# Kernel tuning notes

Measured on AMD Instinct MI355X. Metric: run time of the kernel, lower is better.

## Reference

```python
import jax, jax.numpy as jnp
import numpy as np

B, L, H, E, M = 8, 1024, 1024, 2048, 2048  # batch, seq, hidden_dim, expanded_dim, max_seq_length


def setup_inputs() -> dict:
    key = jax.random.key(0)
    ks = jax.random.split(key, 10)
    n = lambda k, shape, s=0.02: jax.random.normal(k, shape, jnp.float32) * s
    return {
        'x': jax.random.normal(ks[0], (B, L, H), jnp.float32),
        'ln1_w': jnp.ones((H,), jnp.float32), 'ln1_b': jnp.zeros((H,), jnp.float32),
        'ln2_w': jnp.ones((E,), jnp.float32), 'ln2_b': jnp.zeros((E,), jnp.float32),
        'w_qkv': n(ks[1], (3 * E, H)), 'b_qkv': jnp.zeros((3 * E,), jnp.float32),
        'w_out': n(ks[2], (H, E)), 'b_out': jnp.zeros((H,), jnp.float32),
        'rel_pos': n(ks[3], (2 * M - 1, H)),
        'w_beta': n(ks[4], (E, 2 * H)), 'b_beta': jnp.zeros((E,), jnp.float32),
        'w1': n(ks[5], (4 * H, H)), 'b1': jnp.zeros((4 * H,), jnp.float32),
        'w2': n(ks[6], (H, 4 * H)), 'b2': jnp.zeros((H,), jnp.float32),
        'conv_w': n(ks[7], (E, 1, 3), 0.3),  # depthwise conv1d weight [C,1,K]
        'attn_scale': jnp.ones((1,), jnp.float32),
    }


def _ln(x, w, b):
    m = jnp.mean(x, -1, keepdims=True)
    v = jnp.mean((x - m) ** 2, -1, keepdims=True)
    return (x - m) / jnp.sqrt(v + 1e-5) * w + b


def _normalize(x):
    # F.normalize(x, dim=-1): x / max(||x||_2, 1e-12)
    return x / jnp.maximum(jnp.linalg.norm(x, axis=-1, keepdims=True), 1e-12)


def _dwconv(z, w):
    # z: [B,L,E]; depthwise conv1d k=3, pad=1, no bias (groups=E)
    y = jax.lax.conv_general_dilated(
        z.transpose(0, 2, 1), w, window_strides=(1,), padding=((1, 1),),
        feature_group_count=w.shape[0], dimension_numbers=('NCH', 'OIH', 'NCH'))
    return y.transpose(0, 2, 1)


def reference(x, ln1_w, ln1_b, ln2_w, ln2_b, w_qkv, b_qkv, w_out, b_out,
              rel_pos, w_beta, b_beta, w1, b1, w2, b2, conv_w, attn_scale):
    Lx = x.shape[1]
    h = _ln(x, ln1_w, ln1_b)
    qkv = h @ w_qkv.T + b_qkv
    q, k, v = jnp.split(qkv, 3, axis=-1)  # each [B,L,E]
    q = jax.nn.silu(q)
    k = jax.nn.silu(k)
    v = jax.nn.gelu(v, approximate=False)
    # interdependent normalize-mix (k uses the updated q)
    q = _normalize(q) + 0.1 * k
    k = _normalize(k) + 0.1 * q
    q = _dwconv(q, conv_w)
    k = _dwconv(k, conv_w)
    v = _dwconv(v, conv_w)
    # position-conditioned beta gate
    pos_embed = rel_pos[:Lx]  # [L,H]
    pos_info = jnp.einsum('blh,mh->blm', h, pos_embed).mean(-1, keepdims=True)  # [B,L,1]
    comb = jnp.concatenate([h, jnp.broadcast_to(pos_info, h.shape)], axis=-1)  # [B,L,2H]
    beta = jax.nn.sigmoid(comb @ w_beta.T + b_beta) * 0.9 + 0.1  # [B,L,E]
    # delta-rule: state starts at zeros so v_old = state @ k^T = 0 exactly
    v_new = beta * v  # beta*v + (1-beta)*0
    state = jnp.einsum('ble,blf->bef', v_new, k)  # v_new^T @ k : [B,E,E]
    out = jnp.einsum('ble,bfe->blf', q, state) * attn_scale  # q @ state^T
    out = _ln(out, ln2_w, ln2_b) @ w_out.T + b_out
    x = x + out
    h2 = _ln(x, ln1_w, ln1_b)  # norm1 is reused pre-MLP
    mlp = jax.nn.gelu(h2 @ w1.T + b1, approximate=False) @ w2.T + b2
    return x + mlp
```

## Files before the change

### kernel.cpp

```cpp
#include <hip/hip_runtime.h>
#include <hip/hip_bf16.h>
#include <math.h>

using bf16 = __hip_bfloat16;
typedef __attribute__((ext_vector_type(8))) short bf16x8;
typedef __attribute__((ext_vector_type(4))) float f32x4;

#define DEVI __device__ __forceinline__

DEVI float b2f(bf16 v) { return __bfloat162float(v); }
DEVI bf16 f2b(float v) { return __float2bfloat16(v); }
DEVI float geluf(float x) { return 0.5f * x * (1.0f + erff(x * 0.70710678118654752f)); }
DEVI float siluf(float x) { return x / (1.0f + expf(-x)); }

DEVI void load_lds16(const bf16* g, bf16* l) {
  __builtin_amdgcn_global_load_lds(
      (const __attribute__((address_space(1))) void*)g,
      (__attribute__((address_space(3))) void*)l, 16, 0, 0);
}

__global__ __launch_bounds__(256) void cast_kernel(const float* __restrict__ in,
                                                   bf16* __restrict__ out, int n4) {
  int i = blockIdx.x * 256 + threadIdx.x;
  if (i >= n4) return;
  float4 v = reinterpret_cast<const float4*>(in)[i];
  bf16 o[4] = { f2b(v.x), f2b(v.y), f2b(v.z), f2b(v.w) };
  reinterpret_cast<uint2*>(out)[i] = *reinterpret_cast<uint2*>(o);
}

__global__ __launch_bounds__(256) void prep_kernel(const float* __restrict__ rel,
                                                   float* __restrict__ pm,
                                                   const float* __restrict__ wb,
                                                   float* __restrict__ wb2s) {
  const int b = blockIdx.x;
  if (b < 4) {
    int h = b * 256 + threadIdx.x;
    float s = 0.f;
    for (int m = 0; m < 1024; ++m) s += rel[m * 1024 + h];
    pm[h] = s * (1.0f / 1024.0f);
  } else {
    int e = (b - 4) * 4 + (threadIdx.x >> 6);
    int lane = threadIdx.x & 63;
    float s = 0.f;
    for (int j = lane; j < 1024; j += 64) s += wb[(long)e * 2048 + 1024 + j];
#pragma unroll
    for (int off = 32; off > 0; off >>= 1) s += __shfl_down(s, off);
    if (lane == 0) wb2s[e] = s;
  }
}

__global__ __launch_bounds__(256) void convw_pack_kernel(const float* __restrict__ cw,
                                                         bf16* __restrict__ wpl) {
  int e = blockIdx.x * 256 + threadIdx.x;
  wpl[e]        = f2b(cw[e * 3]);
  wpl[2048 + e] = f2b(cw[e * 3 + 1]);
  wpl[4096 + e] = f2b(cw[e * 3 + 2]);
}

template<bool POS>
__global__ __launch_bounds__(256) void ln1024_kernel(
    const float* __restrict__ x, const float* __restrict__ w, const float* __restrict__ b,
    bf16* __restrict__ out, const float* __restrict__ pmean, float* __restrict__ pos) {
  __shared__ float red[12];
  long row = blockIdx.x;
  int t = threadIdx.x, lane = t & 63, wid = t >> 6;
  float4 xv = reinterpret_cast<const float4*>(x + row * 1024)[t];
  float s = xv.x + xv.y + xv.z + xv.w;
  float ss = xv.x * xv.x + xv.y * xv.y + xv.z * xv.z + xv.w * xv.w;
#pragma unroll
  for (int off = 32; off > 0; off >>= 1) { s += __shfl_down(s, off); ss += __shfl_down(ss, off); }
  if (lane == 0) { red[wid] = s; red[4 + wid] = ss; }
  __syncthreads();
  s = red[0] + red[1] + red[2] + red[3];
  ss = red[4] + red[5] + red[6] + red[7];
  float mean = s * (1.0f / 1024.0f);
  float rstd = rsqrtf(ss * (1.0f / 1024.0f) - mean * mean + 1e-5f);
  float4 wv = reinterpret_cast<const float4*>(w)[t];
  float4 bv = reinterpret_cast<const float4*>(b)[t];
  float h0 = (xv.x - mean) * rstd * wv.x + bv.x;
  float h1 = (xv.y - mean) * rstd * wv.y + bv.y;
  float h2 = (xv.z - mean) * rstd * wv.z + bv.z;
  float h3 = (xv.w - mean) * rstd * wv.w + bv.w;
  bf16 o[4] = { f2b(h0), f2b(h1), f2b(h2), f2b(h3) };
  reinterpret_cast<uint2*>(out + row * 1024)[t] = *reinterpret_cast<uint2*>(o);
  if (POS) {
    float4 pv = reinterpret_cast<const float4*>(pmean)[t];
    float d = h0 * pv.x + h1 * pv.y + h2 * pv.z + h3 * pv.w;
#pragma unroll
    for (int off = 32; off > 0; off >>= 1) d += __shfl_down(d, off);
    if (lane == 0) red[8 + wid] = d;
    __syncthreads();
    if (t == 0) pos[row] = red[8] + red[9] + red[10] + red[11];
  }
}

__global__ __launch_bounds__(256) void ln1024b_kernel(
    const bf16* __restrict__ x, const float* __restrict__ w, const float* __restrict__ b,
    bf16* __restrict__ out) {
  __shared__ float red[8];
  long row = blockIdx.x;
  int t = threadIdx.x, lane = t & 63, wid = t >> 6;
  bf16 tv[4];
  *reinterpret_cast<uint2*>(tv) = reinterpret_cast<const uint2*>(x + row * 1024)[t];
  float v[4], s = 0.f, ss = 0.f;
#pragma unroll
  for (int j = 0; j < 4; ++j) { v[j] = b2f(tv[j]); s += v[j]; ss += v[j] * v[j]; }
#pragma unroll
  for (int off = 32; off > 0; off >>= 1) { s += __shfl_down(s, off); ss += __shfl_down(ss, off); }
  if (lane == 0) { red[wid] = s; red[4 + wid] = ss; }
  __syncthreads();
  s = red[0] + red[1] + red[2] + red[3];
  ss = red[4] + red[5] + red[6] + red[7];
  float mean = s * (1.0f / 1024.0f);
  float rstd = rsqrtf(ss * (1.0f / 1024.0f) - mean * mean + 1e-5f);
  float4 wv = reinterpret_cast<const float4*>(w)[t];
  float4 bv = reinterpret_cast<const float4*>(b)[t];
  bf16 o[4];
  o[0] = f2b((v[0] - mean) * rstd * wv.x + bv.x);
  o[1] = f2b((v[1] - mean) * rstd * wv.y + bv.y);
  o[2] = f2b((v[2] - mean) * rstd * wv.z + bv.z);
  o[3] = f2b((v[3] - mean) * rstd * wv.w + bv.w);
  reinterpret_cast<uint2*>(out + row * 1024)[t] = *reinterpret_cast<uint2*>(o);
}

__global__ __launch_bounds__(256) void ln2048_bf16_kernel(
    const bf16* __restrict__ in, const float* __restrict__ w, const float* __restrict__ b,
    bf16* __restrict__ out) {
  __shared__ float red[8];
  long row = blockIdx.x;
  int t = threadIdx.x, lane = t & 63, wid = t >> 6;
  bf16 tv[8];
  *reinterpret_cast<int4*>(tv) = reinterpret_cast<const int4*>(in + row * 2048)[t];
  float v[8], s = 0.f, ss = 0.f;
#pragma unroll
  for (int j = 0; j < 8; ++j) { v[j] = b2f(tv[j]); s += v[j]; ss += v[j] * v[j]; }
#pragma unroll
  for (int off = 32; off > 0; off >>= 1) { s += __shfl_down(s, off); ss += __shfl_down(ss, off); }
  if (lane == 0) { red[wid] = s; red[4 + wid] = ss; }
  __syncthreads();
  s = red[0] + red[1] + red[2] + red[3];
  ss = red[4] + red[5] + red[6] + red[7];
  float mean = s * (1.0f / 2048.0f);
  float rstd = rsqrtf(ss * (1.0f / 2048.0f) - mean * mean + 1e-5f);
  int base = t * 8;
  bf16 o[8];
#pragma unroll
  for (int j = 0; j < 8; ++j) o[j] = f2b((v[j] - mean) * rstd * w[base + j] + b[base + j]);
  reinterpret_cast<int4*>(out + row * 2048)[t] = *reinterpret_cast<int4*>(o);
}

__global__ __launch_bounds__(256) void act_norm_kernel(
    bf16* __restrict__ qp, bf16* __restrict__ kp, bf16* __restrict__ vp) {
  __shared__ float red[8];
  long row = blockIdx.x;
  int t = threadIdx.x, lane = t & 63, wid = t >> 6;
  long ob = row * 2048 + t * 8;
  bf16 tq[8], tk[8], tv[8];
  *reinterpret_cast<int4*>(tq) = *reinterpret_cast<const int4*>(qp + ob);
  *reinterpret_cast<int4*>(tk) = *reinterpret_cast<const int4*>(kp + ob);
  *reinterpret_cast<int4*>(tv) = *reinterpret_cast<const int4*>(vp + ob);
  float qs[8], ks[8];
  float sq = 0.f, sk = 0.f;
#pragma unroll
  for (int j = 0; j < 8; ++j) {
    float q = b2f(tq[j]); qs[j] = siluf(q); sq += qs[j] * qs[j];
    float k = b2f(tk[j]); ks[j] = siluf(k); sk += ks[j] * ks[j];
  }
#pragma unroll
  for (int off = 32; off > 0; off >>= 1) { sq += __shfl_down(sq, off); sk += __shfl_down(sk, off); }
  if (lane == 0) { red[wid] = sq; red[4 + wid] = sk; }
  __syncthreads();
  sq = red[0] + red[1] + red[2] + red[3];
  sk = red[4] + red[5] + red[6] + red[7];
  float rq = 1.0f / fmaxf(sqrtf(sq), 1e-12f);
  float rk = 1.0f / fmaxf(sqrtf(sk), 1e-12f);
  bf16 oq[8], ok[8], ov[8];
#pragma unroll
  for (int j = 0; j < 8; ++j) {
    float qn = qs[j] * rq + 0.1f * ks[j];
    float kn = ks[j] * rk + 0.1f * qn;
    oq[j] = f2b(qn); ok[j] = f2b(kn);
    ov[j] = f2b(geluf(b2f(tv[j])));
  }
  *reinterpret_cast<int4*>(qp + ob) = *reinterpret_cast<int4*>(oq);
  *reinterpret_cast<int4*>(kp + ob) = *reinterpret_cast<int4*>(ok);
  *reinterpret_cast<int4*>(vp + ob) = *reinterpret_cast<int4*>(ov);
}

__global__ __launch_bounds__(256) void dwconv2_kernel(
    const bf16* __restrict__ a_in, bf16* __restrict__ a_out,
    const bf16* __restrict__ b_in, bf16* __restrict__ b_out,
    const bf16* __restrict__ wpl) {
  const bf16* in = blockIdx.y ? b_in : a_in;
  bf16* out = blockIdx.y ? b_out : a_out;
  const int t = threadIdx.x;
  const int e0 = t * 8;
  const long bl = blockIdx.x;
  const int l = (int)(bl & 1023);
  const bf16* mid = in + (bl * 2048 + e0);
  bf16 tm[8], tp[8], tn[8], w0[8], w1[8], w2[8];
  *reinterpret_cast<int4*>(tm) = *reinterpret_cast<const int4*>(mid);
  if (l > 0)    *reinterpret_cast<int4*>(tp) = *reinterpret_cast<const int4*>(mid - 2048);
  if (l < 1023) *reinterpret_cast<int4*>(tn) = *reinterpret_cast<const int4*>(mid + 2048);
  *reinterpret_cast<int4*>(w0) = *reinterpret_cast<const int4*>(&wpl[e0]);
  *reinterpret_cast<int4*>(w1) = *reinterpret_cast<const int4*>(&wpl[2048 + e0]);
  *reinterpret_cast<int4*>(w2) = *reinterpret_cast<const int4*>(&wpl[4096 + e0]);
  bf16 o[8];
#pragma unroll
  for (int j = 0; j < 8; ++j) {
    float a = b2f(w1[j]) * b2f(tm[j]);
    if (l > 0) a += b2f(w0[j]) * b2f(tp[j]);
    if (l < 1023) a += b2f(w2[j]) * b2f(tn[j]);
    o[j] = f2b(a);
  }
  *reinterpret_cast<int4*>(out + (bl * 2048 + e0)) = *reinterpret_cast<int4*>(o);
}

__global__ __launch_bounds__(256) void transpose_kernel(const bf16* __restrict__ in,
                                                        bf16* __restrict__ out) {
  const long base = (long)blockIdx.z * 2097152;
  const int r0 = blockIdx.y * 64 + ((threadIdx.x & 63) >> 3) * 8;
  const int c0 = blockIdx.x * 256 + (threadIdx.x >> 6) * 64 + (threadIdx.x & 7) * 8;
  bf16 v[8][8];
#pragma unroll
  for (int j = 0; j < 8; ++j)
    *reinterpret_cast<int4*>(v[j]) =
        *reinterpret_cast<const int4*>(&in[base + (long)(r0 + j) * 2048 + c0]);
#pragma unroll
  for (int i = 0; i < 8; ++i) {
    bf16 w[8];
#pragma unroll
    for (int j = 0; j < 8; ++j) w[j] = v[j][i];
    *reinterpret_cast<int4*>(&out[base + (long)(c0 + i) * 1024 + r0]) =
        *reinterpret_cast<int4*>(w);
  }
}

enum { EPI_QKV = 0, EPI_BETA = 1, EPI_BF16 = 2, EPI_SCALE = 3, EPI_RES_F32 = 4, EPI_GELU = 5 };

#define MF(d, a, b) d = __builtin_amdgcn_mfma_f32_16x16x32_bf16(a, b, d, 0, 0, 0)
#define RD_A(S, MR, KK) \
  (*reinterpret_cast<const bf16x8*>(&smem[(S)*16384 + wm*8192 + ((MR)*16 + r16)*64 + ((((KK)*32) + kq8) ^ swz)]))
#define RD_B(S, NR, KK) \
  (*reinterpret_cast<const bf16x8*>(&smem[32768 + (S)*16384 + (wn>>1)*8192 + ((wn&1)*64 + (NR)*16 + r16)*64 + ((((KK)*32) + kq8) ^ swz)]))
#define STAGE_A1(S, H, Q, KT) \
  load_lds16(Abase + (long)((H)*128 + (Q)*64) * lda + (long)(KT)*64, \
             &smem[(S)*16384 + (H)*8192 + (Q)*4096 + wid*512])
#define STAGE_B1(S, H, Q, KT) \
  load_lds16(Bbase + (long)((H)*128 + (Q)*64) * ldb + (long)(KT)*64, \
             &smem[32768 + (S)*16384 + (H)*8192 + (Q)*4096 + wid*512])
#define STAGE_AH(S, H, KT) { STAGE_A1(S, H, 0, KT); STAGE_A1(S, H, 1, KT); }
#define STAGE_BH(S, H, KT) { STAGE_B1(S, H, 0, KT); STAGE_B1(S, H, 1, KT); }
#define BAR_A __builtin_amdgcn_s_barrier()
#define LGKM0 { asm volatile("s_waitcnt lgkmcnt(0)" ::: "memory"); __builtin_amdgcn_sched_barrier(0); }
#define VWAIT(LST) { if (LST) { asm volatile("s_waitcnt vmcnt(0)" ::: "memory"); } \
                     else     { asm volatile("s_waitcnt vmcnt(6)" ::: "memory"); } \
                     __builtin_amdgcn_sched_barrier(0); }

#define KTILE(S, ST1, ST2, ST3, ST4, W4) { \
  bf16x8 aL[4][2], aH[4][2], bL[2][2], bH[2][2]; \
  _Pragma("unroll") for (int m_ = 0; m_ < 4; ++m_) { aL[m_][0] = RD_A(S, m_, 0); aL[m_][1] = RD_A(S, m_, 1); } \
  _Pragma("unroll") for (int n_ = 0; n_ < 2; ++n_) { bL[n_][0] = RD_B(S, n_, 0); bL[n_][1] = RD_B(S, n_, 1); } \
  ST1; BAR_A; LGKM0; \
  __builtin_amdgcn_s_setprio(1); \
  _Pragma("unroll") for (int m_ = 0; m_ < 4; ++m_) _Pragma("unroll") for (int n_ = 0; n_ < 2; ++n_) { \
    MF(acc[m_][n_], aL[m_][0], bL[n_][0]); MF(acc[m_][n_], aL[m_][1], bL[n_][1]); } \
  __builtin_amdgcn_s_setprio(0); __builtin_amdgcn_s_barrier(); \
  _Pragma("unroll") for (int n_ = 0; n_ < 2; ++n_) { bH[n_][0] = RD_B(S, n_ + 2, 0); bH[n_][1] = RD_B(S, n_ + 2, 1); } \
  ST2; BAR_A; LGKM0; \
  __builtin_amdgcn_s_setprio(1); \
  _Pragma("unroll") for (int m_ = 0; m_ < 4; ++m_) _Pragma("unroll") for (int n_ = 0; n_ < 2; ++n_) { \
    MF(acc[m_][n_ + 2], aL[m_][0], bH[n_][0]); MF(acc[m_][n_ + 2], aL[m_][1], bH[n_][1]); } \
  __builtin_amdgcn_s_setprio(0); __builtin_amdgcn_s_barrier(); \
  _Pragma("unroll") for (int m_ = 0; m_ < 4; ++m_) { aH[m_][0] = RD_A(S, m_ + 4, 0); aH[m_][1] = RD_A(S, m_ + 4, 1); } \
  ST3; BAR_A; LGKM0; \
  __builtin_amdgcn_s_setprio(1); \
  _Pragma("unroll") for (int m_ = 0; m_ < 4; ++m_) _Pragma("unroll") for (int n_ = 0; n_ < 2; ++n_) { \
    MF(acc[m_ + 4][n_], aH[m_][0], bL[n_][0]); MF(acc[m_ + 4][n_], aH[m_][1], bL[n_][1]); } \
  __builtin_amdgcn_s_setprio(0); __builtin_amdgcn_s_barrier(); \
  ST4; W4; BAR_A; LGKM0; \
  __builtin_amdgcn_s_setprio(1); \
  _Pragma("unroll") for (int m_ = 0; m_ < 4; ++m_) _Pragma("unroll") for (int n_ = 0; n_ < 2; ++n_) { \
    MF(acc[m_ + 4][n_ + 2], aH[m_][0], bH[n_][0]); MF(acc[m_ + 4][n_ + 2], aH[m_][1], bH[n_][1]); } \
  __builtin_amdgcn_s_setprio(0); __builtin_amdgcn_s_barrier(); \
}

template<int EPI>
__global__ __launch_bounds__(512) void gemm256_kernel(
    const bf16* __restrict__ A, int lda, long sA,
    const bf16* __restrict__ B, int ldb, long sB,
    void* __restrict__ Cv, int ldc, long sC, int K,
    const float* __restrict__ bias, const float* __restrict__ aux_row,
    const float* __restrict__ aux_col, const bf16* __restrict__ vconv,
    const float* __restrict__ resid, const float* __restrict__ scale_ptr,
    bf16* __restrict__ p2, bf16* __restrict__ p3) {
  __shared__ bf16 smem[65536];
  const int bz = blockIdx.z;
  A += (long)bz * sA;
  B += (long)bz * sB;
  const int m0 = blockIdx.y * 256, n0 = blockIdx.x * 256;
  const int t = threadIdx.x, lane = t & 63, wid = t >> 6;
  const int wm = wid >> 2, wn = wid & 3;
  const int r16 = lane & 15, kq8 = (lane >> 4) * 8;
  const int swz = (r16 & 7) << 3;
  const int lrow = lane >> 3;
  const int cswz = ((lane & 7) ^ lrow) * 8;
  const bf16* Abase = A + (long)(m0 + wid * 8 + lrow) * lda + cswz;
  const bf16* Bbase = B + (long)(n0 + wid * 8 + lrow) * ldb + cswz;
  f32x4 acc[8][4] = {};
  const int NT = K >> 6, NIT = NT >> 1;
  STAGE_AH(0, 0, 0); STAGE_AH(0, 1, 0); STAGE_BH(0, 0, 0); STAGE_BH(0, 1, 0);
  STAGE_BH(1, 0, 1); STAGE_BH(1, 1, 1); STAGE_AH(1, 0, 1);
  asm volatile("s_waitcnt vmcnt(6)" ::: "memory");
  __builtin_amdgcn_sched_barrier(0);
  __builtin_amdgcn_s_barrier();
  for (int i = 0; i < NIT; ++i) {
    const int tb = 2 * i;
    const bool lst = (i == NIT - 1);
    KTILE(0,
      { STAGE_AH(1, 1, tb + 1); },
      { },
      { if (!lst) { STAGE_BH(0, 0, tb + 2); STAGE_BH(0, 1, tb + 2); } },
      { if (!lst) { STAGE_AH(0, 0, tb + 2); } },
      VWAIT(lst));
    KTILE(1,
      { if (!lst) { STAGE_AH(0, 1, tb + 2); } },
      { },
      { if (!lst) { STAGE_BH(1, 0, tb + 3); STAGE_BH(1, 1, tb + 3); } },
      { if (!lst) { STAGE_AH(1, 0, tb + 3); } },
      VWAIT(lst));
  }
  float scl = 1.0f;
  if (EPI == EPI_SCALE) scl = scale_ptr[0];
  const int rb = (lane >> 4) * 4;
#pragma unroll
  for (int mr = 0; mr < 8; ++mr) {
#pragma unroll
    for (int nr = 0; nr < 4; ++nr) {
#pragma unroll
      for (int r = 0; r < 4; ++r) {
        const long gm = m0 + wm * 128 + mr * 16 + rb + r;
        const int gn = n0 + wn * 64 + nr * 16 + r16;
        const long idx = (long)bz * sC + gm * (long)ldc + gn;
        float v = acc[mr][nr][r];
        if (EPI == EPI_QKV) {
          const int seg = gn >> 11, cc = gn & 2047;
          bf16* dst = (seg == 0) ? (bf16*)Cv : (seg == 1) ? p2 : p3;
          dst[gm * 2048 + cc] = f2b(v + bias[gn]);
        } else if (EPI == EPI_BETA) {
          float tt = v + bias[gn] + aux_row[gm] * aux_col[gn];
          float be = 0.9f / (1.0f + expf(-tt)) + 0.1f;
          ((bf16*)Cv)[idx] = f2b(be * b2f(vconv[idx]));
        } else if (EPI == EPI_BF16) {
          ((bf16*)Cv)[idx] = f2b(v);
        } else if (EPI == EPI_SCALE) {
          ((bf16*)Cv)[idx] = f2b(v * scl);
        } else if (EPI == EPI_RES_F32) {
          ((float*)Cv)[idx] = v + bias[gn] + resid[idx];
        } else {
          ((bf16*)Cv)[idx] = f2b(geluf(v + bias[gn]));
        }
      }
    }
  }
}

#define A_RD(S, MR, KK) \
  (*reinterpret_cast<const bf16x8*>(&amem[(S)*8192 + (wm*64 + (MR)*16 + r16)*64 + ((((KK)*32) + kq8) ^ swz)]))
#define B_RD(S, NR, KK) \
  (*reinterpret_cast<const bf16x8*>(&amem[16384 + (S)*16384 + (wn*64 + (NR)*16 + r16)*64 + ((((KK)*32) + kq8) ^ swz)]))
#define A_ST(S, Q, KT) \
  load_lds16(Abase + (long)((Q)*64) * lda + (long)(KT)*64, &amem[(S)*8192 + (Q)*4096 + wid*512])
#define B_ST(S, Q, KT) \
  load_lds16(Bbase + (long)((Q)*64) * ldb + (long)(KT)*64, &amem[16384 + (S)*16384 + (Q)*4096 + wid*512])
#define STAGE_T(S, KT) { A_ST(S, 0, KT); A_ST(S, 1, KT); B_ST(S, 0, KT); B_ST(S, 1, KT); B_ST(S, 2, KT); B_ST(S, 3, KT); }

template<int RB, int WB, int NR>
__global__ __launch_bounds__(512) void gemmA128_kernel(
    const bf16* __restrict__ A, int lda, long sA,
    const bf16* __restrict__ B, int ldb, long sB,
    void* __restrict__ Cv, int ldc, long sC, int K,
    const float* __restrict__ bias, const void* __restrict__ residv) {
  __shared__ bf16 amem[49152];
  A += (long)blockIdx.z * sA;
  B += (long)blockIdx.z * sB;
  const int m0 = blockIdx.y * 128, n0 = blockIdx.x * 256;
  const int t = threadIdx.x, lane = t & 63, wid = t >> 6;
  const int wm = wid >> 2, wn = wid & 3;
  const int r16 = lane & 15, kq8 = (lane >> 4) * 8;
  const int swz = (r16 & 7) << 3;
  const int lrow = lane >> 3;
  const int cswz = ((lane & 7) ^ lrow) * 8;
  const bf16* Abase = A + (long)(m0 + wid * 8 + lrow) * lda + cswz;
  const bf16* Bbase = B + (long)(n0 + wid * 8 + lrow) * ldb + cswz;
  f32x4 acc[4][4] = {};
  const int NT = K >> 6;
  STAGE_T(0, 0); STAGE_T(1, 1);
  asm volatile("s_waitcnt vmcnt(6)" ::: "memory");
  __builtin_amdgcn_sched_barrier(0);
  __builtin_amdgcn_s_barrier();
  for (int tt = 0; tt < NT; ++tt) {
    const int S = tt & 1;
    const bool pre = (tt + 2 < NT);
    bf16x8 a[4][2], bL[2][2], bH[2][2];
#pragma unroll
    for (int m_ = 0; m_ < 4; ++m_) { a[m_][0] = A_RD(S, m_, 0); a[m_][1] = A_RD(S, m_, 1); }
#pragma unroll
    for (int n_ = 0; n_ < 2; ++n_) { bL[n_][0] = B_RD(S, n_, 0); bL[n_][1] = B_RD(S, n_, 1); }
#pragma unroll
    for (int n_ = 0; n_ < 2; ++n_) { bH[n_][0] = B_RD(S, n_ + 2, 0); bH[n_][1] = B_RD(S, n_ + 2, 1); }
    LGKM0;
    __builtin_amdgcn_s_setprio(1);
#pragma unroll
    for (int m_ = 0; m_ < 4; ++m_)
#pragma unroll
      for (int n_ = 0; n_ < 2; ++n_) {
        MF(acc[m_][n_], a[m_][0], bL[n_][0]); MF(acc[m_][n_], a[m_][1], bL[n_][1]);
      }
    __builtin_amdgcn_s_setprio(0);
    __builtin_amdgcn_s_barrier();
    __builtin_amdgcn_sched_barrier(0);
    if (pre) STAGE_T(S, tt + 2);
    __builtin_amdgcn_s_setprio(1);
#pragma unroll
    for (int m_ = 0; m_ < 4; ++m_)
#pragma unroll
      for (int n_ = 0; n_ < 2; ++n_) {
        MF(acc[m_][n_ + 2], a[m_][0], bH[n_][0]); MF(acc[m_][n_ + 2], a[m_][1], bH[n_][1]);
      }
    __builtin_amdgcn_s_setprio(0);
    if (pre) { asm volatile("s_waitcnt vmcnt(6)" ::: "memory"); }
    else     { asm volatile("s_waitcnt vmcnt(0)" ::: "memory"); }
    __builtin_amdgcn_sched_barrier(0);
    __builtin_amdgcn_s_barrier();
    __builtin_amdgcn_sched_barrier(0);
  }
  const int rb = (lane >> 4) * 4;
#pragma unroll
  for (int mr = 0; mr < 4; ++mr) {
#pragma unroll
    for (int nr = 0; nr < 4; ++nr) {
#pragma unroll
      for (int r = 0; r < 4; ++r) {
        const long gm = m0 + wm * 64 + mr * 16 + rb + r;
        const int gn = n0 + wn * 64 + nr * 16 + r16;
        const long idx = (long)blockIdx.z * sC + gm * (long)ldc + gn;
        float o = acc[mr][nr][r];
        if (!NR) {
          o += bias[gn];
          o += RB ? b2f(((const bf16*)residv)[idx]) : ((const float*)residv)[idx];
        }
        if (WB) ((bf16*)Cv)[idx] = f2b(o);
        else    ((float*)Cv)[idx] = o;
      }
    }
  }
}

extern "C" void kernel_launch(void* const* d_in, const int* in_sizes, int n_in,
                              void* d_out, int out_size, void* d_ws, size_t ws_size,
                              hipStream_t stream) {
  (void)in_sizes; (void)n_in; (void)out_size;
  const float* x       = (const float*)d_in[0];
  const float* ln1_w   = (const float*)d_in[1];
  const float* ln1_b   = (const float*)d_in[2];
  const float* ln2_w   = (const float*)d_in[3];
  const float* ln2_b   = (const float*)d_in[4];
  const float* w_qkv   = (const float*)d_in[5];
  const float* b_qkv   = (const float*)d_in[6];
  const float* w_out   = (const float*)d_in[7];
  const float* b_out   = (const float*)d_in[8];
  const float* rel_pos = (const float*)d_in[9];
  const float* w_beta  = (const float*)d_in[10];
  const float* b_beta  = (const float*)d_in[11];
  const float* w1      = (const float*)d_in[12];
  const float* b1      = (const float*)d_in[13];
  const float* w2      = (const float*)d_in[14];
  const float* b2      = (const float*)d_in[15];
  const float* conv_w  = (const float*)d_in[16];
  const float* attn_sc = (const float*)d_in[17];
  float* out = (float*)d_out;

  if (ws_size < 180400128UL) return;
  char* ws = (char*)d_ws;
  bf16*  wbuf    = (bf16*)(ws + 0);
  bf16*  wpl     = (bf16*)(ws + 11534336UL);
  float* pmean   = (float*)(ws + 12582912UL);
  float* wb2s    = (float*)(ws + 12587008UL);
  float* posinfo = (float*)(ws + 12595200UL);
  bf16* R0 = (bf16*)(ws + 12627968UL);
  bf16* R1 = (bf16*)(ws + 46182400UL);
  bf16* R2 = (bf16*)(ws + 79736832UL);
  bf16* R3 = (bf16*)(ws + 113291264UL);
  bf16* R4 = (bf16*)(ws + 146845696UL);
  bf16* vscr = (bf16*)d_out;
  bf16* x2b = R1;

  prep_kernel<<<516, 256, 0, stream>>>(rel_pos, pmean, w_beta, wb2s);

  ln1024_kernel<true><<<8192, 256, 0, stream>>>(x, ln1_w, ln1_b, R0, pmean, posinfo);

  cast_kernel<<<6144, 256, 0, stream>>>(w_qkv, wbuf, 1572864);
  gemm256_kernel<EPI_QKV><<<dim3(24, 32, 1), 512, 0, stream>>>(
      R0, 1024, 0, wbuf, 1024, 0, R1, 2048, 0, 1024,
      b_qkv, nullptr, nullptr, nullptr, nullptr, nullptr, R2, R3);

  act_norm_kernel<<<8192, 256, 0, stream>>>(R1, R2, R3);

  convw_pack_kernel<<<8, 256, 0, stream>>>(conv_w, wpl);
  dwconv2_kernel<<<dim3(8192, 2), 256, 0, stream>>>(R1, R4, R3, vscr, wpl);

  cast_kernel<<<4096, 256, 0, stream>>>(w_beta, wbuf, 1048576);
  gemm256_kernel<EPI_BETA><<<dim3(8, 32, 1), 512, 0, stream>>>(
      R0, 1024, 0, wbuf, 2048, 0, R1, 2048, 0, 1024,
      b_beta, posinfo, wb2s, vscr, nullptr, nullptr, nullptr, nullptr);

  dwconv2_kernel<<<dim3(8192, 1), 256, 0, stream>>>(R2, R3, R2, R3, wpl);

  transpose_kernel<<<dim3(8, 16, 8), 256, 0, stream>>>(R1, R0);

  gemmA128_kernel<0, 1, 1><<<dim3(4, 8, 8), 512, 0, stream>>>(
      R4, 2048, 2097152, R3, 2048, 2097152, R2, 1024, 1048576, 2048,
      nullptr, nullptr);

  gemm256_kernel<EPI_SCALE><<<dim3(8, 4, 8), 512, 0, stream>>>(
      R2, 1024, 1048576, R0, 1024, 2097152, R3, 2048, 2097152, 1024,
      nullptr, nullptr, nullptr, nullptr, nullptr, attn_sc, nullptr, nullptr);

  ln2048_bf16_kernel<<<8192, 256, 0, stream>>>(R3, ln2_w, ln2_b, R0);

  cast_kernel<<<2048, 256, 0, stream>>>(w_out, wbuf, 524288);
  gemmA128_kernel<0, 1, 0><<<dim3(4, 64, 1), 512, 0, stream>>>(
      R0, 2048, 0, wbuf, 2048, 0, x2b, 1024, 0, 2048, b_out, x);

  ln1024b_kernel<<<8192, 256, 0, stream>>>(x2b, ln1_w, ln1_b, R2);

  cast_kernel<<<4096, 256, 0, stream>>>(w1, wbuf, 1048576);
  gemm256_kernel<EPI_GELU><<<dim3(16, 32, 1), 512, 0, stream>>>(
      R2, 1024, 0, wbuf, 1024, 0, R3, 4096, 0, 1024,
      b1, nullptr, nullptr, nullptr, nullptr, nullptr, nullptr, nullptr);

  cast_kernel<<<4096, 256, 0, stream>>>(w2, wbuf, 1048576);
  gemmA128_kernel<1, 0, 0><<<dim3(4, 64, 1), 512, 0, stream>>>(
      R3, 4096, 0, wbuf, 4096, 0, out, 1024, 0, 4096, b2, x2b);
}
```

Baseline: 685.8 us.

## Fuse activation/normalize into depthwise conv with halo row recomputation

Removes the separate act_norm pass and the dwconv passes by recomputing silu/normalize/mix (and gelu for v) for the three neighbouring rows inside each conv block. Intermediate activated q/k/v no longer round-trip through global memory, and two launches are eliminated. In exchange, each block reads three rows of q and k and recomputes the activation math and row reductions three times. Bf16 rounding of intermediates is kept to match the earlier numerics.

```diff
diff --git a/kernel.cpp b/kernel.cpp
--- a/kernel.cpp
+++ b/kernel.cpp
@@ -149,71 +149,137 @@
   reinterpret_cast<int4*>(out + row * 2048)[t] = *reinterpret_cast<int4*>(o);
 }
 
-__global__ __launch_bounds__(256) void act_norm_kernel(
-    bf16* __restrict__ qp, bf16* __restrict__ kp, bf16* __restrict__ vp) {
-  __shared__ float red[8];
-  long row = blockIdx.x;
-  int t = threadIdx.x, lane = t & 63, wid = t >> 6;
-  long ob = row * 2048 + t * 8;
-  bf16 tq[8], tk[8], tv[8];
-  *reinterpret_cast<int4*>(tq) = *reinterpret_cast<const int4*>(qp + ob);
-  *reinterpret_cast<int4*>(tk) = *reinterpret_cast<const int4*>(kp + ob);
-  *reinterpret_cast<int4*>(tv) = *reinterpret_cast<const int4*>(vp + ob);
-  float qs[8], ks[8];
-  float sq = 0.f, sk = 0.f;
-#pragma unroll
-  for (int j = 0; j < 8; ++j) {
-    float q = b2f(tq[j]); qs[j] = siluf(q); sq += qs[j] * qs[j];
-    float k = b2f(tk[j]); ks[j] = siluf(k); sk += ks[j] * ks[j];
-  }
-#pragma unroll
-  for (int off = 32; off > 0; off >>= 1) { sq += __shfl_down(sq, off); sk += __shfl_down(sk, off); }
-  if (lane == 0) { red[wid] = sq; red[4 + wid] = sk; }
-  __syncthreads();
-  sq = red[0] + red[1] + red[2] + red[3];
-  sk = red[4] + red[5] + red[6] + red[7];
-  float rq = 1.0f / fmaxf(sqrtf(sq), 1e-12f);
-  float rk = 1.0f / fmaxf(sqrtf(sk), 1e-12f);
-  bf16 oq[8], ok[8], ov[8];
-#pragma unroll
-  for (int j = 0; j < 8; ++j) {
-    float qn = qs[j] * rq + 0.1f * ks[j];
-    float kn = ks[j] * rk + 0.1f * qn;
-    oq[j] = f2b(qn); ok[j] = f2b(kn);
-    ov[j] = f2b(geluf(b2f(tv[j])));
-  }
-  *reinterpret_cast<int4*>(qp + ob) = *reinterpret_cast<int4*>(oq);
-  *reinterpret_cast<int4*>(kp + ob) = *reinterpret_cast<int4*>(ok);
-  *reinterpret_cast<int4*>(vp + ob) = *reinterpret_cast<int4*>(ov);
-}
-
-__global__ __launch_bounds__(256) void dwconv2_kernel(
-    const bf16* __restrict__ a_in, bf16* __restrict__ a_out,
-    const bf16* __restrict__ b_in, bf16* __restrict__ b_out,
-    const bf16* __restrict__ wpl) {
-  const bf16* in = blockIdx.y ? b_in : a_in;
-  bf16* out = blockIdx.y ? b_out : a_out;
+
+__global__ __launch_bounds__(256) void actconv_qv_kernel(
+    const bf16* __restrict__ qraw, const bf16* __restrict__ kraw, bf16* __restrict__ qout,
+    const bf16* __restrict__ vraw, bf16* __restrict__ vout, const bf16* __restrict__ wpl) {
+  const long bl = blockIdx.x;
+  const int l = (int)(bl & 1023);
   const int t = threadIdx.x;
   const int e0 = t * 8;
+  bf16 w0[8], w1[8], w2[8];
+  *reinterpret_cast<int4*>(w0) = *reinterpret_cast<const int4*>(wpl + e0);
+  *reinterpret_cast<int4*>(w1) = *reinterpret_cast<const int4*>(wpl + 2048 + e0);
+  *reinterpret_cast<int4*>(w2) = *reinterpret_cast<const int4*>(wpl + 4096 + e0);
+  if (blockIdx.y == 1) {
+    const long mid = bl * 2048 + e0;
+    bf16 tm[8], tp[8], tn[8];
+    *reinterpret_cast<int4*>(tm) = *reinterpret_cast<const int4*>(vraw + mid);
+    if (l > 0)    *reinterpret_cast<int4*>(tp) = *reinterpret_cast<const int4*>(vraw + mid - 2048);
+    if (l < 1023) *reinterpret_cast<int4*>(tn) = *reinterpret_cast<const int4*>(vraw + mid + 2048);
+    bf16 o[8];
+#pragma unroll
+    for (int j = 0; j < 8; ++j) {
+      float a = b2f(w1[j]) * b2f(f2b(geluf(b2f(tm[j]))));
+      if (l > 0)    a += b2f(w0[j]) * b2f(f2b(geluf(b2f(tp[j]))));
+      if (l < 1023) a += b2f(w2[j]) * b2f(f2b(geluf(b2f(tn[j]))));
+      o[j] = f2b(a);
+    }
+    *reinterpret_cast<int4*>(vout + mid) = *reinterpret_cast<int4*>(o);
+    return;
+  }
+  __shared__ float red[3][2][4];
+  const int lane = t & 63, wid = t >> 6;
+  float qs[3][8], ks[3][8], rq[3];
+#pragma unroll
+  for (int rr = 0; rr < 3; ++rr) {
+    int dl = l + rr - 1;
+    float sq = 0.f, sk = 0.f;
+    if (dl >= 0 && dl < 1024) {
+      long off = (bl + rr - 1) * 2048 + e0;
+      bf16 tq[8], tk[8];
+      *reinterpret_cast<int4*>(tq) = *reinterpret_cast<const int4*>(qraw + off);
+      *reinterpret_cast<int4*>(tk) = *reinterpret_cast<const int4*>(kraw + off);
+#pragma unroll
+      for (int j = 0; j < 8; ++j) {
+        float q = b2f(tq[j]); qs[rr][j] = siluf(q); sq += qs[rr][j] * qs[rr][j];
+        float k = b2f(tk[j]); ks[rr][j] = siluf(k); sk += ks[rr][j] * ks[rr][j];
+      }
+    } else {
+#pragma unroll
+      for (int j = 0; j < 8; ++j) { qs[rr][j] = 0.f; ks[rr][j] = 0.f; }
+    }
+#pragma unroll
+    for (int off = 32; off > 0; off >>= 1) { sq += __shfl_down(sq, off); sk += __shfl_down(sk, off); }
+    if (lane == 0) { red[rr][0][wid] = sq; red[rr][1][wid] = sk; }
+  }
+  __syncthreads();
+#pragma unroll
+  for (int rr = 0; rr < 3; ++rr) {
+    float sq = red[rr][0][0] + red[rr][0][1] + red[rr][0][2] + red[rr][0][3];
+    rq[rr] = 1.0f / fmaxf(sqrtf(sq), 1e-12f);
+  }
+  bf16 o[8];
+#pragma unroll
+  for (int j = 0; j < 8; ++j) {
+    float a = b2f(w1[j]) * b2f(f2b(qs[1][j] * rq[1] + 0.1f * ks[1][j]));
+    if (l > 0)    a += b2f(w0[j]) * b2f(f2b(qs[0][j] * rq[0] + 0.1f * ks[0][j]));
+    if (l < 1023) a += b2f(w2[j]) * b2f(f2b(qs[2][j] * rq[2] + 0.1f * ks[2][j]));
+    o[j] = f2b(a);
+  }
+  *reinterpret_cast<int4*>(qout + bl * 2048 + e0) = *reinterpret_cast<int4*>(o);
+}
+
+__global__ __launch_bounds__(256) void actconv_k_kernel(
+    const bf16* __restrict__ qraw, const bf16* __restrict__ kraw, bf16* __restrict__ kout,
+    const bf16* __restrict__ wpl) {
   const long bl = blockIdx.x;
   const int l = (int)(bl & 1023);
-  const bf16* mid = in + (bl * 2048 + e0);
-  bf16 tm[8], tp[8], tn[8], w0[8], w1[8], w2[8];
-  *reinterpret_cast<int4*>(tm) = *reinterpret_cast<const int4*>(mid);
-  if (l > 0)    *reinterpret_cast<int4*>(tp) = *reinterpret_cast<const int4*>(mid - 2048);
-  if (l < 1023) *reinterpret_cast<int4*>(tn) = *reinterpret_cast<const int4*>(mid + 2048);
-  *reinterpret_cast<int4*>(w0) = *reinterpret_cast<const int4*>(&wpl[e0]);
-  *reinterpret_cast<int4*>(w1) = *reinterpret_cast<const int4*>(&wpl[2048 + e0]);
-  *reinterpret_cast<int4*>(w2) = *reinterpret_cast<const int4*>(&wpl[4096 + e0]);
+  const int t = threadIdx.x;
+  const int e0 = t * 8;
+  __shared__ float red[3][2][4];
+  const int lane = t & 63, wid = t >> 6;
+  float qs[3][8], ks[3][8], rq[3], rk[3];
+#pragma unroll
+  for (int rr = 0; rr < 3; ++rr) {
+    int dl = l + rr - 1;
+    float sq = 0.f, sk = 0.f;
+    if (dl >= 0 && dl < 1024) {
+      long off = (bl + rr - 1) * 2048 + e0;
+      bf16 tq[8], tk[8];
+      *reinterpret_cast<int4*>(tq) = *reinterpret_cast<const int4*>(qraw + off);
+      *reinterpret_cast<int4*>(tk) = *reinterpret_cast<const int4*>(kraw + off);
+#pragma unroll
+      for (int j = 0; j < 8; ++j) {
+        float q = b2f(tq[j]); qs[rr][j] = siluf(q); sq += qs[rr][j] * qs[rr][j];
+        float k = b2f(tk[j]); ks[rr][j] = siluf(k); sk += ks[rr][j] * ks[rr][j];
+      }
+    } else {
+#pragma unroll
+      for (int j = 0; j < 8; ++j) { qs[rr][j] = 0.f; ks[rr][j] = 0.f; }
+    }
+#pragma unroll
+    for (int off = 32; off > 0; off >>= 1) { sq += __shfl_down(sq, off); sk += __shfl_down(sk, off); }
+    if (lane == 0) { red[rr][0][wid] = sq; red[rr][1][wid] = sk; }
+  }
+  __syncthreads();
+#pragma unroll
+  for (int rr = 0; rr < 3; ++rr) {
+    float sq = red[rr][0][0] + red[rr][0][1] + red[rr][0][2] + red[rr][0][3];
+    float sk = red[rr][1][0] + red[rr][1][1] + red[rr][1][2] + red[rr][1][3];
+    rq[rr] = 1.0f / fmaxf(sqrtf(sq), 1e-12f);
+    rk[rr] = 1.0f / fmaxf(sqrtf(sk), 1e-12f);
+  }
+  bf16 w0[8], w1[8], w2[8];
+  *reinterpret_cast<int4*>(w0) = *reinterpret_cast<const int4*>(wpl + e0);
+  *reinterpret_cast<int4*>(w1) = *reinterpret_cast<const int4*>(wpl + 2048 + e0);
+  *reinterpret_cast<int4*>(w2) = *reinterpret_cast<const int4*>(wpl + 4096 + e0);
   bf16 o[8];
 #pragma unroll
   for (int j = 0; j < 8; ++j) {
-    float a = b2f(w1[j]) * b2f(tm[j]);
-    if (l > 0) a += b2f(w0[j]) * b2f(tp[j]);
-    if (l < 1023) a += b2f(w2[j]) * b2f(tn[j]);
+    float qn1 = qs[1][j] * rq[1] + 0.1f * ks[1][j];
+    float a = b2f(w1[j]) * b2f(f2b(ks[1][j] * rk[1] + 0.1f * qn1));
+    if (l > 0) {
+      float qn0 = qs[0][j] * rq[0] + 0.1f * ks[0][j];
+      a += b2f(w0[j]) * b2f(f2b(ks[0][j] * rk[0] + 0.1f * qn0));
+    }
+    if (l < 1023) {
+      float qn2 = qs[2][j] * rq[2] + 0.1f * ks[2][j];
+      a += b2f(w2[j]) * b2f(f2b(ks[2][j] * rk[2] + 0.1f * qn2));
+    }
     o[j] = f2b(a);
   }
-  *reinterpret_cast<int4*>(out + (bl * 2048 + e0)) = *reinterpret_cast<int4*>(o);
+  *reinterpret_cast<int4*>(kout + bl * 2048 + e0) = *reinterpret_cast<int4*>(o);
 }
 
 __global__ __launch_bounds__(256) void transpose_kernel(const bf16* __restrict__ in,
@@ -505,18 +571,16 @@
       R0, 1024, 0, wbuf, 1024, 0, R1, 2048, 0, 1024,
       b_qkv, nullptr, nullptr, nullptr, nullptr, nullptr, R2, R3);
 
-  act_norm_kernel<<<8192, 256, 0, stream>>>(R1, R2, R3);
-
   convw_pack_kernel<<<8, 256, 0, stream>>>(conv_w, wpl);
-  dwconv2_kernel<<<dim3(8192, 2), 256, 0, stream>>>(R1, R4, R3, vscr, wpl);
+
+  actconv_qv_kernel<<<dim3(8192, 2), 256, 0, stream>>>(R1, R2, R4, R3, vscr, wpl);
+  actconv_k_kernel<<<8192, 256, 0, stream>>>(R1, R2, R3, wpl);
 
   cast_kernel<<<4096, 256, 0, stream>>>(w_beta, wbuf, 1048576);
   gemm256_kernel<EPI_BETA><<<dim3(8, 32, 1), 512, 0, stream>>>(
       R0, 1024, 0, wbuf, 2048, 0, R1, 2048, 0, 1024,
       b_beta, posinfo, wb2s, vscr, nullptr, nullptr, nullptr, nullptr);
 
-  dwconv2_kernel<<<dim3(8192, 1), 256, 0, stream>>>(R2, R3, R2, R3, wpl);
-
   transpose_kernel<<<dim3(8, 16, 8), 256, 0, stream>>>(R1, R0);
 
   gemmA128_kernel<0, 1, 1><<<dim3(4, 8, 8), 512, 0, stream>>>(
```

Result: slower. 792.5 us (+15.6%).

## Fuse q/k/v activation and normalize-mix into depthwise conv kernels

Applied to the files above, without the earlier changes.

Drops the separate activation/normalize kernel and the later conv passes. New kernels read raw q/k/v, apply silu or gelu plus the row-norm mix in registers for an 8-row tile with a one-row halo, and write conv outputs directly. This removes several full read/write passes over the [B,L,E] bf16 tensors and a few launches. In exchange, halo rows are recomputed (10 rows per 8 outputs), each block now holds 10 rows of q and k in registers, and silu uses the fast __expf.

```diff
diff --git a/kernel.cpp b/kernel.cpp
--- a/kernel.cpp
+++ b/kernel.cpp
@@ -10,8 +10,14 @@
 
 DEVI float b2f(bf16 v) { return __bfloat162float(v); }
 DEVI bf16 f2b(float v) { return __float2bfloat16(v); }
+DEVI short b2s(bf16 v) { return *reinterpret_cast<short*>(&v); }
+DEVI float s2f(short s) {
+  unsigned int u = ((unsigned int)(unsigned short)s) << 16;
+  return __uint_as_float(u);
+}
 DEVI float geluf(float x) { return 0.5f * x * (1.0f + erff(x * 0.70710678118654752f)); }
 DEVI float siluf(float x) { return x / (1.0f + expf(-x)); }
+DEVI float fsilu(float x) { return x / (1.0f + __expf(-x)); }
 
 DEVI void load_lds16(const bf16* g, bf16* l) {
   __builtin_amdgcn_global_load_lds(
@@ -149,71 +155,115 @@
   reinterpret_cast<int4*>(out + row * 2048)[t] = *reinterpret_cast<int4*>(o);
 }
 
-__global__ __launch_bounds__(256) void act_norm_kernel(
-    bf16* __restrict__ qp, bf16* __restrict__ kp, bf16* __restrict__ vp) {
-  __shared__ float red[8];
-  long row = blockIdx.x;
-  int t = threadIdx.x, lane = t & 63, wid = t >> 6;
-  long ob = row * 2048 + t * 8;
-  bf16 tq[8], tk[8], tv[8];
-  *reinterpret_cast<int4*>(tq) = *reinterpret_cast<const int4*>(qp + ob);
-  *reinterpret_cast<int4*>(tk) = *reinterpret_cast<const int4*>(kp + ob);
-  *reinterpret_cast<int4*>(tv) = *reinterpret_cast<const int4*>(vp + ob);
-  float qs[8], ks[8];
-  float sq = 0.f, sk = 0.f;
-#pragma unroll
-  for (int j = 0; j < 8; ++j) {
-    float q = b2f(tq[j]); qs[j] = siluf(q); sq += qs[j] * qs[j];
-    float k = b2f(tk[j]); ks[j] = siluf(k); sk += ks[j] * ks[j];
-  }
-#pragma unroll
-  for (int off = 32; off > 0; off >>= 1) { sq += __shfl_down(sq, off); sk += __shfl_down(sk, off); }
-  if (lane == 0) { red[wid] = sq; red[4 + wid] = sk; }
+
+#define QK_TAP(RR, WV) { \
+  float qmv = s2f(qs[RR][j]), kmv = s2f(ks[RR][j]); \
+  float qn = qmv * rq[RR] + 0.1f * kmv; \
+  float kn = kmv * rk[RR] + 0.1f * qn; \
+  accq += b2f(WV[j]) * b2f(f2b(qn)); \
+  acck += b2f(WV[j]) * b2f(f2b(kn)); }
+
+__global__ __launch_bounds__(256) void actconv_qk_kernel(
+    const bf16* __restrict__ qraw, const bf16* __restrict__ kraw,
+    bf16* __restrict__ qout, bf16* __restrict__ kout, const bf16* __restrict__ wpl) {
+  __shared__ float red[10][2][4];
+  const int t = threadIdx.x, lane = t & 63, wid = t >> 6;
+  const int e0 = t * 8;
+  const int bb = blockIdx.x >> 7;
+  const int l0 = (blockIdx.x & 127) * 8;
+  const long rowbase = (long)bb * 1024 * 2048;
+  bf16x8 qs[10], ks[10];
+#pragma unroll
+  for (int r = 0; r < 10; ++r) {
+    int dl = l0 + r - 1;
+    float sq = 0.f, sk = 0.f;
+    if (dl >= 0 && dl < 1024) {
+      long off = rowbase + (long)dl * 2048 + e0;
+      bf16 tq[8], tk[8];
+      *reinterpret_cast<int4*>(tq) = *reinterpret_cast<const int4*>(qraw + off);
+      *reinterpret_cast<int4*>(tk) = *reinterpret_cast<const int4*>(kraw + off);
+#pragma unroll
+      for (int j = 0; j < 8; ++j) {
+        float qv = fsilu(b2f(tq[j])); sq += qv * qv; qs[r][j] = b2s(f2b(qv));
+        float kv = fsilu(b2f(tk[j])); sk += kv * kv; ks[r][j] = b2s(f2b(kv));
+      }
+    } else {
+      qs[r] = 0; ks[r] = 0;
+    }
+#pragma unroll
+    for (int off = 32; off > 0; off >>= 1) { sq += __shfl_down(sq, off); sk += __shfl_down(sk, off); }
+    if (lane == 0) { red[r][0][wid] = sq; red[r][1][wid] = sk; }
+  }
   __syncthreads();
-  sq = red[0] + red[1] + red[2] + red[3];
-  sk = red[4] + red[5] + red[6] + red[7];
-  float rq = 1.0f / fmaxf(sqrtf(sq), 1e-12f);
-  float rk = 1.0f / fmaxf(sqrtf(sk), 1e-12f);
-  bf16 oq[8], ok[8], ov[8];
-#pragma unroll
-  for (int j = 0; j < 8; ++j) {
-    float qn = qs[j] * rq + 0.1f * ks[j];
-    float kn = ks[j] * rk + 0.1f * qn;
-    oq[j] = f2b(qn); ok[j] = f2b(kn);
-    ov[j] = f2b(geluf(b2f(tv[j])));
-  }
-  *reinterpret_cast<int4*>(qp + ob) = *reinterpret_cast<int4*>(oq);
-  *reinterpret_cast<int4*>(kp + ob) = *reinterpret_cast<int4*>(ok);
-  *reinterpret_cast<int4*>(vp + ob) = *reinterpret_cast<int4*>(ov);
-}
-
-__global__ __launch_bounds__(256) void dwconv2_kernel(
-    const bf16* __restrict__ a_in, bf16* __restrict__ a_out,
-    const bf16* __restrict__ b_in, bf16* __restrict__ b_out,
-    const bf16* __restrict__ wpl) {
-  const bf16* in = blockIdx.y ? b_in : a_in;
-  bf16* out = blockIdx.y ? b_out : a_out;
+  float rq[10], rk[10];
+#pragma unroll
+  for (int r = 0; r < 10; ++r) {
+    float sq = red[r][0][0] + red[r][0][1] + red[r][0][2] + red[r][0][3];
+    float sk = red[r][1][0] + red[r][1][1] + red[r][1][2] + red[r][1][3];
+    rq[r] = 1.0f / fmaxf(sqrtf(sq), 1e-12f);
+    rk[r] = 1.0f / fmaxf(sqrtf(sk), 1e-12f);
+  }
+  bf16 w0[8], w1[8], w2[8];
+  *reinterpret_cast<int4*>(w0) = *reinterpret_cast<const int4*>(wpl + e0);
+  *reinterpret_cast<int4*>(w1) = *reinterpret_cast<const int4*>(wpl + 2048 + e0);
+  *reinterpret_cast<int4*>(w2) = *reinterpret_cast<const int4*>(wpl + 4096 + e0);
+#pragma unroll
+  for (int rr = 1; rr <= 8; ++rr) {
+    const int l = l0 + rr - 1;
+    bf16 oq[8], ok[8];
+#pragma unroll
+    for (int j = 0; j < 8; ++j) {
+      float accq = 0.f, acck = 0.f;
+      QK_TAP(rr, w1);
+      if (l > 0)    QK_TAP(rr - 1, w0);
+      if (l < 1023) QK_TAP(rr + 1, w2);
+      oq[j] = f2b(accq); ok[j] = f2b(acck);
+    }
+    long off = rowbase + (long)l * 2048 + e0;
+    *reinterpret_cast<int4*>(qout + off) = *reinterpret_cast<int4*>(oq);
+    *reinterpret_cast<int4*>(kout + off) = *reinterpret_cast<int4*>(ok);
+  }
+}
+
+__global__ __launch_bounds__(256) void actconv_v_kernel(
+    const bf16* __restrict__ vraw, bf16* __restrict__ vout, const bf16* __restrict__ wpl) {
   const int t = threadIdx.x;
   const int e0 = t * 8;
-  const long bl = blockIdx.x;
-  const int l = (int)(bl & 1023);
-  const bf16* mid = in + (bl * 2048 + e0);
-  bf16 tm[8], tp[8], tn[8], w0[8], w1[8], w2[8];
-  *reinterpret_cast<int4*>(tm) = *reinterpret_cast<const int4*>(mid);
-  if (l > 0)    *reinterpret_cast<int4*>(tp) = *reinterpret_cast<const int4*>(mid - 2048);
-  if (l < 1023) *reinterpret_cast<int4*>(tn) = *reinterpret_cast<const int4*>(mid + 2048);
-  *reinterpret_cast<int4*>(w0) = *reinterpret_cast<const int4*>(&wpl[e0]);
-  *reinterpret_cast<int4*>(w1) = *reinterpret_cast<const int4*>(&wpl[2048 + e0]);
-  *reinterpret_cast<int4*>(w2) = *reinterpret_cast<const int4*>(&wpl[4096 + e0]);
-  bf16 o[8];
-#pragma unroll
-  for (int j = 0; j < 8; ++j) {
-    float a = b2f(w1[j]) * b2f(tm[j]);
-    if (l > 0) a += b2f(w0[j]) * b2f(tp[j]);
-    if (l < 1023) a += b2f(w2[j]) * b2f(tn[j]);
-    o[j] = f2b(a);
-  }
-  *reinterpret_cast<int4*>(out + (bl * 2048 + e0)) = *reinterpret_cast<int4*>(o);
+  const int bb = blockIdx.x >> 7;
+  const int l0 = (blockIdx.x & 127) * 8;
+  const long rowbase = (long)bb * 1024 * 2048;
+  bf16x8 vs[10];
+#pragma unroll
+  for (int r = 0; r < 10; ++r) {
+    int dl = l0 + r - 1;
+    if (dl >= 0 && dl < 1024) {
+      bf16 tvv[8];
+      *reinterpret_cast<int4*>(tvv) =
+          *reinterpret_cast<const int4*>(vraw + rowbase + (long)dl * 2048 + e0);
+#pragma unroll
+      for (int j = 0; j < 8; ++j) vs[r][j] = b2s(f2b(geluf(b2f(tvv[j]))));
+    } else {
+      vs[r] = 0;
+    }
+  }
+  bf16 w0[8], w1[8], w2[8];
+  *reinterpret_cast<int4*>(w0) = *reinterpret_cast<const int4*>(wpl + e0);
+  *reinterpret_cast<int4*>(w1) = *reinterpret_cast<const int4*>(wpl + 2048 + e0);
+  *reinterpret_cast<int4*>(w2) = *reinterpret_cast<const int4*>(wpl + 4096 + e0);
+#pragma unroll
+  for (int rr = 1; rr <= 8; ++rr) {
+    const int l = l0 + rr - 1;
+    bf16 ov[8];
+#pragma unroll
+    for (int j = 0; j < 8; ++j) {
+      float a = b2f(w1[j]) * s2f(vs[rr][j]);
+      if (l > 0)    a += b2f(w0[j]) * s2f(vs[rr - 1][j]);
+      if (l < 1023) a += b2f(w2[j]) * s2f(vs[rr + 1][j]);
+      ov[j] = f2b(a);
+    }
+    *reinterpret_cast<int4*>(vout + rowbase + (long)l * 2048 + e0) =
+        *reinterpret_cast<int4*>(ov);
+  }
 }
 
 __global__ __launch_bounds__(256) void transpose_kernel(const bf16* __restrict__ in,
@@ -503,19 +553,17 @@
   cast_kernel<<<6144, 256, 0, stream>>>(w_qkv, wbuf, 1572864);
   gemm256_kernel<EPI_QKV><<<dim3(24, 32, 1), 512, 0, stream>>>(
       R0, 1024, 0, wbuf, 1024, 0, R1, 2048, 0, 1024,
-      b_qkv, nullptr, nullptr, nullptr, nullptr, nullptr, R2, R3);
-
-  act_norm_kernel<<<8192, 256, 0, stream>>>(R1, R2, R3);
+      b_qkv, nullptr, nullptr, nullptr, nullptr, nullptr, R2, vscr);
 
   convw_pack_kernel<<<8, 256, 0, stream>>>(conv_w, wpl);
-  dwconv2_kernel<<<dim3(8192, 2), 256, 0, stream>>>(R1, R4, R3, vscr, wpl);
+
+  actconv_qk_kernel<<<1024, 256, 0, stream>>>(R1, R2, R4, R3, wpl);
+  actconv_v_kernel<<<1024, 256, 0, stream>>>(vscr, R1, wpl);
 
   cast_kernel<<<4096, 256, 0, stream>>>(w_beta, wbuf, 1048576);
   gemm256_kernel<EPI_BETA><<<dim3(8, 32, 1), 512, 0, stream>>>(
       R0, 1024, 0, wbuf, 2048, 0, R1, 2048, 0, 1024,
-      b_beta, posinfo, wb2s, vscr, nullptr, nullptr, nullptr, nullptr);
-
-  dwconv2_kernel<<<dim3(8192, 1), 256, 0, stream>>>(R2, R3, R2, R3, wpl);
+      b_beta, posinfo, wb2s, R1, nullptr, nullptr, nullptr, nullptr);
 
   transpose_kernel<<<dim3(8, 16, 8), 256, 0, stream>>>(R1, R0);
 
```

Measured after the change: 654.9 us. -4.5%, faster.
